# Performance work log

Hardware: AMD Instinct MI355X
Metric: run time of the kernel (lower is better)

Reference implementation:

```python
import jax, jax.numpy as jnp
import numpy as np

DMODEL = 1024
HEADS = 16
KEY_DIM = DMODEL // HEADS


def setup_inputs() -> dict:
    key = jax.random.key(0)
    k0, k1, k2, k3, k4 = jax.random.split(key, 5)
    scale = 1.0 / np.sqrt(DMODEL)
    return {
        "inputs": jax.random.normal(k0, (2, 2048, DMODEL), dtype=jnp.float32),
        "Wq": jax.random.normal(k1, (DMODEL, DMODEL), dtype=jnp.float32) * scale,
        "Wk": jax.random.normal(k2, (DMODEL, DMODEL), dtype=jnp.float32) * scale,
        "Wv": jax.random.normal(k3, (DMODEL, DMODEL), dtype=jnp.float32) * scale,
        "Wo": jax.random.normal(k4, (DMODEL, DMODEL), dtype=jnp.float32) * scale,
    }


def reference(inputs, Wq, Wk, Wv, Wo):
    B, S, _ = inputs.shape
    # nn.Linear(bias=False): y = x @ W.T ; then reshape to (B, S, H, Dh) and transpose to (B, H, S, Dh)
    def proj(W):
        return (inputs @ W.T).reshape(B, S, HEADS, KEY_DIM).transpose(0, 2, 1, 3)

    q, k, v = proj(Wq), proj(Wk), proj(Wv)
    scale = 1.0 / np.sqrt(KEY_DIM).astype(np.float32)
    score = jnp.einsum('bhsd,bhtd->bhst', q, k) * scale  # [B,H,S,S]
    attn = jax.nn.softmax(score, axis=-1)
    out = jnp.einsum('bhst,bhtd->bhsd', attn, v)  # [B,H,S,Dh]
    out = out.transpose(0, 2, 1, 3).reshape(B, S, HEADS * KEY_DIM)
    return out @ Wo.T
```

## Files before the change

### kernel.cpp

```cpp
#include <hip/hip_runtime.h>
#include <hip/hip_bf16.h>
#include <stdint.h>

typedef __attribute__((ext_vector_type(8))) short short8;
typedef __attribute__((ext_vector_type(4))) float floatx4;

#define MFMA16(a, b, c) __builtin_amdgcn_mfma_f32_16x16x32_bf16((a), (b), (c), 0, 0, 0)

static __device__ __forceinline__ uint16_t f2bf(float f) {
  union { float f; uint32_t u; } x; x.f = f;
  uint32_t r = x.u + 0x7fffu + ((x.u >> 16) & 1u);
  return (uint16_t)(r >> 16);
}

static __device__ __forceinline__ uint32_t cvtpk_bf16(float lo, float hi) {
  uint32_t r;
  asm("v_cvt_pk_bf16_f32 %0, %1, %2" : "=v"(r) : "v"(lo), "v"(hi));
  return r;
}

constexpr int DM = 1024, NH = 16, KD = 64, NB = 2, SQ = 2048;
constexpr int MTOT = NB * SQ;
constexpr int NT = SQ / 64;

__global__ void convert_kernel(const float* __restrict__ X,
                               const float* __restrict__ Wq, const float* __restrict__ Wk,
                               const float* __restrict__ Wv, const float* __restrict__ Wo,
                               uint16_t* __restrict__ Xb, uint16_t* __restrict__ Wqkvb,
                               uint16_t* __restrict__ Wob) {
  const int NX = MTOT * DM;
  const int NW = DM * DM;
  const int TOT8 = (NX + 4 * NW) / 8;
  for (int t = blockIdx.x * blockDim.x + threadIdx.x; t < TOT8; t += gridDim.x * blockDim.x) {
    int i = t * 8;
    const float* src; uint16_t* dst;
    if (i < NX) { src = X + i; dst = Xb + i; }
    else if (i < NX + 3 * NW) {
      int j = i - NX; dst = Wqkvb + j;
      src = (j < NW) ? (Wq + j) : (j < 2 * NW) ? (Wk + (j - NW)) : (Wv + (j - 2 * NW));
    } else {
      int j = i - NX - 3 * NW; src = Wo + j; dst = Wob + j;
    }
    float4 a = ((const float4*)src)[0];
    float4 b = ((const float4*)src)[1];
    ushort4 o0, o1;
    o0.x = f2bf(a.x); o0.y = f2bf(a.y); o0.z = f2bf(a.z); o0.w = f2bf(a.w);
    o1.x = f2bf(b.x); o1.y = f2bf(b.y); o1.z = f2bf(b.z); o1.w = f2bf(b.w);
    ((ushort4*)dst)[0] = o0;
    ((ushort4*)dst)[1] = o1;
  }
}

template <int MODE>
__global__ __launch_bounds__(256) void gemm_bt(const uint16_t* __restrict__ Aq,
                                               const uint16_t* __restrict__ Bq, int Ntiles,
                                               uint16_t* __restrict__ Qb, uint16_t* __restrict__ Kb,
                                               uint16_t* __restrict__ VTb, float* __restrict__ Out) {
  __shared__ uint16_t Al[128 * 32];
  __shared__ uint16_t Bl[128 * 32];
  const int K = 1024;
  int nwg = gridDim.x;
  int bid = (blockIdx.x & 7) * (nwg >> 3) + (blockIdx.x >> 3);
  int bm = bid / Ntiles, bn = bid % Ntiles;
  int brow = bm * 128, bcol = bn * 128;
  int tid = threadIdx.x;
  int w = tid >> 6, lane = tid & 63, g = lane >> 4, c16 = lane & 15;
  int wm = w >> 1, wn = w & 1;
  int rr = tid >> 2;
  int ce = (tid & 3) * 8;

  floatx4 acc[4][4] = {};

  for (int k0 = 0; k0 < K; k0 += 32) {
    __syncthreads();
#pragma unroll
    for (int c = 0; c < 2; ++c) {
      __builtin_amdgcn_global_load_lds(
          (const __attribute__((address_space(1))) void*)(Aq + (size_t)(brow + c * 64 + rr) * K + k0 + ce),
          (__attribute__((address_space(3))) void*)((char*)Al + c * 4096 + w * 1024), 16, 0, 0);
      __builtin_amdgcn_global_load_lds(
          (const __attribute__((address_space(1))) void*)(Bq + (size_t)(bcol + c * 64 + rr) * K + k0 + ce),
          (__attribute__((address_space(3))) void*)((char*)Bl + c * 4096 + w * 1024), 16, 0, 0);
    }
    __syncthreads();
    short8 af[4], bf[4];
#pragma unroll
    for (int mt = 0; mt < 4; ++mt)
      af[mt] = *(const short8*)&Al[(wm * 64 + mt * 16 + c16) * 32 + g * 8];
#pragma unroll
    for (int nt = 0; nt < 4; ++nt)
      bf[nt] = *(const short8*)&Bl[(wn * 64 + nt * 16 + c16) * 32 + g * 8];
#pragma unroll
    for (int mt = 0; mt < 4; ++mt)
#pragma unroll
      for (int nt = 0; nt < 4; ++nt)
        acc[mt][nt] = MFMA16(af[mt], bf[nt], acc[mt][nt]);
  }

#pragma unroll
  for (int mt = 0; mt < 4; ++mt) {
#pragma unroll
    for (int nt = 0; nt < 4; ++nt) {
      int n = bcol + wn * 64 + nt * 16 + c16;
#pragma unroll
      for (int r = 0; r < 4; ++r) {
        int m = brow + wm * 64 + mt * 16 + g * 4 + r;
        float v = acc[mt][nt][r];
        if (MODE == 0) {
          int proj = n >> 10;
          int hd = n & 1023;
          int h = hd >> 6, d = hd & 63;
          int b = m >> 11, s = m & 2047;
          size_t bh = (size_t)(b * NH + h);
          if (proj == 0) {
            Qb[(bh * SQ + s) * KD + d] = f2bf(v * 0.18033688011112042f);
          } else if (proj == 1) {
            int st = s >> 4, r2 = s & 15, k8 = d >> 3, j = d & 7;
            Kb[bh * (size_t)(SQ * KD) + (((size_t)(st * 8 + k8) * 16 + r2) * 8 + j)] = f2bf(v);
          } else {
            int kt = s >> 6, kvl = s & 63;
            int c = kvl >> 5, tth = (kvl >> 4) & 1, gg = (kvl >> 2) & 3, rs = kvl & 3;
            int jp = tth * 4 + rs;
            int dt = d >> 4, cc = d & 15;
            VTb[bh * (size_t)(SQ * KD) + (size_t)kt * 4096 +
                (size_t)((c * 4 + dt) * 512 + gg * 128 + cc * 8 + jp)] = f2bf(v);
          }
        } else {
          Out[(size_t)m * DM + n] = v;
        }
      }
    }
  }
}

__global__ __launch_bounds__(256, 4) void attn_kernel(const uint16_t* __restrict__ Q,
                                                      const uint16_t* __restrict__ Kt,
                                                      const uint16_t* __restrict__ Vt,
                                                      uint16_t* __restrict__ O) {
  int bid = blockIdx.x;
  int bh = bid & 31, qt = bid >> 5;
  int qb = qt * 64;
  int b = bh >> 4, h = bh & 15;
  int tid = threadIdx.x, w = tid >> 6, lane = tid & 63, g = lane >> 4, c16 = lane & 15;

  const uint16_t* Qh = Q + (size_t)bh * SQ * KD;
  const uint16_t* Kh = Kt + (size_t)bh * SQ * KD;
  const uint16_t* Vh = Vt + (size_t)bh * SQ * KD;

  int qrow = qb + w * 16 + c16;
  short8 qf0 = *(const short8*)&Qh[(size_t)qrow * KD + g * 8];
  short8 qf1 = *(const short8*)&Qh[(size_t)qrow * KD + 32 + g * 8];

  float m = -1e30f, l = 0.0f;
  floatx4 accO[4] = {};

  short8 kfb[2][4][2];
#define LOADK(buf, tile)                                                              \
  {                                                                                   \
    const uint16_t* kt_ = Kh + (size_t)(tile) * 4096;                                 \
    _Pragma("unroll") for (int tt = 0; tt < 4; ++tt)                                  \
        _Pragma("unroll") for (int hf = 0; hf < 2; ++hf)                              \
            kfb[buf][tt][hf] = *(const short8*)&kt_[tt * 1024 + hf * 512 + lane * 8]; \
  }

  LOADK(0, 0);

#pragma unroll 2
  for (int t = 0; t < NT; ++t) {
    int cur = t & 1;

    short8 vf[2][4];
    const uint16_t* vtile = Vh + (size_t)t * 4096;
#pragma unroll
    for (int c = 0; c < 2; ++c)
#pragma unroll
      for (int dt = 0; dt < 4; ++dt)
        vf[c][dt] = *(const short8*)&vtile[(c * 4 + dt) * 512 + lane * 8];

    floatx4 sacc[4] = {};
#pragma unroll
    for (int tt = 0; tt < 4; ++tt) {
      sacc[tt] = MFMA16(kfb[cur][tt][0], qf0, sacc[tt]);
      sacc[tt] = MFMA16(kfb[cur][tt][1], qf1, sacc[tt]);
    }

    LOADK(cur ^ 1, (t + 1 < NT) ? (t + 1) : t);

    float mx = fmaxf(fmaxf(fmaxf(sacc[0][0], sacc[0][1]), fmaxf(sacc[0][2], sacc[0][3])),
                     fmaxf(fmaxf(sacc[1][0], sacc[1][1]), fmaxf(sacc[1][2], sacc[1][3])));
    mx = fmaxf(mx, fmaxf(fmaxf(fmaxf(sacc[2][0], sacc[2][1]), fmaxf(sacc[2][2], sacc[2][3])),
                         fmaxf(fmaxf(sacc[3][0], sacc[3][1]), fmaxf(sacc[3][2], sacc[3][3]))));
    mx = fmaxf(mx, __shfl_xor(mx, 16));
    mx = fmaxf(mx, __shfl_xor(mx, 32));
    if (!__all(mx <= m + 8.0f)) {
      float nm = fmaxf(m, mx);
      float al = exp2f(m - nm);
      m = nm;
      l *= al;
      float av[4];
#pragma unroll
      for (int r = 0; r < 4; ++r) av[r] = __shfl(al, g * 4 + r);
#pragma unroll
      for (int dt = 0; dt < 4; ++dt)
#pragma unroll
        for (int r = 0; r < 4; ++r) accO[dt][r] *= av[r];
    }
    float ss = 0.0f;
#pragma unroll
    for (int tt = 0; tt < 4; ++tt) {
#pragma unroll
      for (int r = 0; r < 4; ++r)
        sacc[tt][r] = exp2f(sacc[tt][r] - m);
      ss += (sacc[tt][0] + sacc[tt][1]) + (sacc[tt][2] + sacc[tt][3]);
    }
    ss += __shfl_xor(ss, 16);
    ss += __shfl_xor(ss, 32);
    l += ss;

    union { uint32_t u[4]; short8 s8; } pa[2];
#pragma unroll
    for (int c = 0; c < 2; ++c) {
      pa[c].u[0] = cvtpk_bf16(sacc[2 * c][0], sacc[2 * c][1]);
      pa[c].u[1] = cvtpk_bf16(sacc[2 * c][2], sacc[2 * c][3]);
      pa[c].u[2] = cvtpk_bf16(sacc[2 * c + 1][0], sacc[2 * c + 1][1]);
      pa[c].u[3] = cvtpk_bf16(sacc[2 * c + 1][2], sacc[2 * c + 1][3]);
    }
#pragma unroll
    for (int c = 0; c < 2; ++c)
#pragma unroll
      for (int dt = 0; dt < 4; ++dt)
        accO[dt] = MFMA16(pa[c].s8, vf[c][dt], accO[dt]);
  }
#undef LOADK

  float lv[4];
#pragma unroll
  for (int r = 0; r < 4; ++r) lv[r] = 1.0f / __shfl(l, g * 4 + r);
#pragma unroll
  for (int dt = 0; dt < 4; ++dt) {
#pragma unroll
    for (int r = 0; r < 4; ++r) {
      int s = qb + w * 16 + g * 4 + r;
      int d = dt * 16 + c16;
      O[((size_t)(b * SQ + s)) * DM + h * KD + d] = f2bf(accO[dt][r] * lv[r]);
    }
  }
}

extern "C" void kernel_launch(void* const* d_in, const int* in_sizes, int n_in,
                              void* d_out, int out_size, void* d_ws, size_t ws_size,
                              hipStream_t stream) {
  const float* X = (const float*)d_in[0];
  const float* Wq = (const float*)d_in[1];
  const float* Wk = (const float*)d_in[2];
  const float* Wv = (const float*)d_in[3];
  const float* Wo = (const float*)d_in[4];
  float* out = (float*)d_out;

  char* ws = (char*)d_ws;
  uint16_t* Xb    = (uint16_t*)(ws);
  uint16_t* Wqkvb = (uint16_t*)(ws + 8388608);
  uint16_t* Wob   = (uint16_t*)(ws + 14680064);
  uint16_t* Qb    = (uint16_t*)(ws + 16777216);
  uint16_t* Kb    = (uint16_t*)(ws + 25165824);
  uint16_t* VTb   = (uint16_t*)(ws + 33554432);
  uint16_t* Ob    = (uint16_t*)(ws + 41943040);

  hipLaunchKernelGGL(convert_kernel, dim3(1024), dim3(256), 0, stream,
                     X, Wq, Wk, Wv, Wo, Xb, Wqkvb, Wob);
  hipLaunchKernelGGL((gemm_bt<0>), dim3(32 * 24), dim3(256), 0, stream,
                     Xb, Wqkvb, 24, Qb, Kb, VTb, nullptr);
  hipLaunchKernelGGL(attn_kernel, dim3(1024), dim3(256), 0, stream,
                     Qb, Kb, VTb, Ob);
  hipLaunchKernelGGL((gemm_bt<1>), dim3(32 * 8), dim3(256), 0, stream,
                     Ob, Wob, 8, nullptr, nullptr, nullptr, out);
}
```

Before: 215.4 us.

## Prefetch V across iterations, set MFMA priority, defer row-sum reduction

The attention loop now prefetches the next V tile after the PV MFMAs, using single K and V register buffers. It no longer loads V at the top of each iteration or double-buffers K. The MFMA blocks are wrapped in s_setprio raises so waves doing matrix math are favoured. The per-iteration cross-lane shuffle reduction of the softmax row sum is moved out of the loop into a single reduction at the end. This is valid because the rescale factor is uniform across the lanes being combined. Together these aim to hide load latency and cut shuffle work, though loading into the same buffer right after use may add register dependencies that stall.

```diff
diff --git a/kernel.cpp b/kernel.cpp
--- a/kernel.cpp
+++ b/kernel.cpp
@@ -141,50 +141,53 @@
   int bh = bid & 31, qt = bid >> 5;
   int qb = qt * 64;
   int b = bh >> 4, h = bh & 15;
-  int tid = threadIdx.x, w = tid >> 6, lane = tid & 63, g = lane >> 4, c16 = lane & 15;
+  int tid = threadIdx.x, lane = tid & 63, wv = tid >> 6, g = lane >> 4, c16 = lane & 15;
 
   const uint16_t* Qh = Q + (size_t)bh * SQ * KD;
   const uint16_t* Kh = Kt + (size_t)bh * SQ * KD;
   const uint16_t* Vh = Vt + (size_t)bh * SQ * KD;
 
-  int qrow = qb + w * 16 + c16;
+  int qrow = qb + wv * 16 + c16;
   short8 qf0 = *(const short8*)&Qh[(size_t)qrow * KD + g * 8];
   short8 qf1 = *(const short8*)&Qh[(size_t)qrow * KD + 32 + g * 8];
 
   float m = -1e30f, l = 0.0f;
   floatx4 accO[4] = {};
 
-  short8 kfb[2][4][2];
-#define LOADK(buf, tile)                                                              \
-  {                                                                                   \
-    const uint16_t* kt_ = Kh + (size_t)(tile) * 4096;                                 \
-    _Pragma("unroll") for (int tt = 0; tt < 4; ++tt)                                  \
-        _Pragma("unroll") for (int hf = 0; hf < 2; ++hf)                              \
-            kfb[buf][tt][hf] = *(const short8*)&kt_[tt * 1024 + hf * 512 + lane * 8]; \
-  }
-
-  LOADK(0, 0);
-
-#pragma unroll 2
+  short8 kf[4][2];
+  short8 vf[2][4];
+
+#define LOADK(tile)                                                                 \
+  {                                                                                 \
+    const uint16_t* kt_ = Kh + (size_t)(tile) * 4096;                               \
+    _Pragma("unroll") for (int tt = 0; tt < 4; ++tt)                                \
+        _Pragma("unroll") for (int hf = 0; hf < 2; ++hf)                            \
+            kf[tt][hf] = *(const short8*)&kt_[tt * 1024 + hf * 512 + lane * 8];     \
+  }
+#define LOADV(tile)                                                                 \
+  {                                                                                 \
+    const uint16_t* vt_ = Vh + (size_t)(tile) * 4096;                               \
+    _Pragma("unroll") for (int c = 0; c < 2; ++c)                                   \
+        _Pragma("unroll") for (int dt = 0; dt < 4; ++dt)                            \
+            vf[c][dt] = *(const short8*)&vt_[(c * 4 + dt) * 512 + lane * 8];        \
+  }
+
+  LOADK(0);
+  LOADV(0);
+
   for (int t = 0; t < NT; ++t) {
-    int cur = t & 1;
-
-    short8 vf[2][4];
-    const uint16_t* vtile = Vh + (size_t)t * 4096;
-#pragma unroll
-    for (int c = 0; c < 2; ++c)
-#pragma unroll
-      for (int dt = 0; dt < 4; ++dt)
-        vf[c][dt] = *(const short8*)&vtile[(c * 4 + dt) * 512 + lane * 8];
+    int tn = (t + 1 < NT) ? (t + 1) : t;
 
     floatx4 sacc[4] = {};
+    __builtin_amdgcn_s_setprio(1);
 #pragma unroll
     for (int tt = 0; tt < 4; ++tt) {
-      sacc[tt] = MFMA16(kfb[cur][tt][0], qf0, sacc[tt]);
-      sacc[tt] = MFMA16(kfb[cur][tt][1], qf1, sacc[tt]);
-    }
-
-    LOADK(cur ^ 1, (t + 1 < NT) ? (t + 1) : t);
+      sacc[tt] = MFMA16(kf[tt][0], qf0, sacc[tt]);
+      sacc[tt] = MFMA16(kf[tt][1], qf1, sacc[tt]);
+    }
+    __builtin_amdgcn_s_setprio(0);
+
+    LOADK(tn);
 
     float mx = fmaxf(fmaxf(fmaxf(sacc[0][0], sacc[0][1]), fmaxf(sacc[0][2], sacc[0][3])),
                      fmaxf(fmaxf(sacc[1][0], sacc[1][1]), fmaxf(sacc[1][2], sacc[1][3])));
@@ -209,12 +212,11 @@
 #pragma unroll
     for (int tt = 0; tt < 4; ++tt) {
 #pragma unroll
-      for (int r = 0; r < 4; ++r)
+      for (int r = 0; r < 4; ++r) {
         sacc[tt][r] = exp2f(sacc[tt][r] - m);
-      ss += (sacc[tt][0] + sacc[tt][1]) + (sacc[tt][2] + sacc[tt][3]);
-    }
-    ss += __shfl_xor(ss, 16);
-    ss += __shfl_xor(ss, 32);
+        ss += sacc[tt][r];
+      }
+    }
     l += ss;
 
     union { uint32_t u[4]; short8 s8; } pa[2];
@@ -225,13 +227,21 @@
       pa[c].u[2] = cvtpk_bf16(sacc[2 * c + 1][0], sacc[2 * c + 1][1]);
       pa[c].u[3] = cvtpk_bf16(sacc[2 * c + 1][2], sacc[2 * c + 1][3]);
     }
+    __builtin_amdgcn_s_setprio(1);
 #pragma unroll
     for (int c = 0; c < 2; ++c)
 #pragma unroll
       for (int dt = 0; dt < 4; ++dt)
         accO[dt] = MFMA16(pa[c].s8, vf[c][dt], accO[dt]);
+    __builtin_amdgcn_s_setprio(0);
+
+    LOADV(tn);
   }
 #undef LOADK
+#undef LOADV
+
+  l += __shfl_xor(l, 16);
+  l += __shfl_xor(l, 32);
 
   float lv[4];
 #pragma unroll
@@ -240,7 +250,7 @@
   for (int dt = 0; dt < 4; ++dt) {
 #pragma unroll
     for (int r = 0; r < 4; ++r) {
-      int s = qb + w * 16 + g * 4 + r;
+      int s = qb + wv * 16 + g * 4 + r;
       int d = dt * 16 + c16;
       O[((size_t)(b * SQ + s)) * DM + h * KD + d] = f2bf(accO[dt][r] * lv[r]);
     }
```

New measurement: 215.6 us. About the same (+0.1%).
